# Performance work log

Measured on AMD Instinct MI355X. Metric: run time of the kernel, lower is better.

The kernel has to match this reference:

```python
import jax, jax.numpy as jnp
import numpy as np

B, N, D = 4, 4096, 256
DENSITY = 0.02


def setup_inputs() -> dict:
    key = jax.random.key(0)
    kx, ka1, ka2, kwt, kbt, kwh, kth = jax.random.split(key, 7)
    x = jax.random.normal(kx, (B, N, D), dtype=jnp.float32)
    # sparse weighted adjacency, materialized densely for the reference
    mask = jax.random.uniform(ka1, (B, N, N)) < DENSITY
    vals = jax.random.uniform(ka2, (B, N, N), dtype=jnp.float32)
    adj = jnp.where(mask, vals, 0.0).astype(jnp.float32)
    s = 0.02  # random_normal initializer stddev
    W_t = s * jax.random.normal(kwt, (D, D), dtype=jnp.float32)
    b_t = s * jax.random.normal(kbt, (D,), dtype=jnp.float32)
    W_h = s * jax.random.normal(kwh, (D, D), dtype=jnp.float32)
    theta = s * jax.random.normal(kth, (D, D), dtype=jnp.float32)
    return {"x": x, "adj": adj, "W_t": W_t, "b_t": b_t, "W_h": W_h, "theta": theta}


def reference(x, adj, W_t, b_t, W_h, theta):
    # degree normalization: norm = (deg + 1e-6)^{-1/2}
    in_degrees = jnp.sum(adj, axis=-1)                      # [B, N]
    norm = jnp.power(in_degrees + 1e-6, -0.5)[..., None]    # [B, N, 1]
    # homophilic path: D^{-1/2} A D^{-1/2} (x theta)
    f_hom = jnp.einsum('bnd,de->bne', x, theta) * norm      # [B, N, D]
    f_hom = jnp.einsum('bnm,bmd->bnd', adj, f_hom) * norm   # batched SpMM (dense ref)
    # heterophilic path
    f_het = jnp.einsum('bnd,de->bne', x, W_h)
    # gate and fuse
    gate = jax.nn.sigmoid(jnp.einsum('bnd,de->bne', x, W_t) + b_t)
    out = gate * f_hom + (1.0 - gate) * f_het
    return jax.nn.elu(out)
```

## Files before the change

kernel.cpp:

```cpp
#include <hip/hip_runtime.h>
#include <math.h>

constexpr int Nn = 4096;
constexpr int Dd = 256;
constexpr int Mrows = 16384;
constexpr int CAP = 192;
constexpr int GEMM_BLOCKS = 768;

typedef __attribute__((ext_vector_type(8))) short short8;
typedef __attribute__((ext_vector_type(4))) float f32x4;

__device__ __forceinline__ unsigned short f2bf(float f) {
    unsigned int u = __float_as_uint(f);
    u = (u + 0x7FFFu + ((u >> 16) & 1u)) >> 16;
    return (unsigned short)u;
}
__device__ __forceinline__ float bf2f(unsigned short u) {
    return __uint_as_float((unsigned int)u << 16);
}

__global__ __launch_bounds__(256) void prep_kernel(
    const float* __restrict__ x, const float* __restrict__ theta,
    const float* __restrict__ Wh, const float* __restrict__ Wt,
    unsigned short* __restrict__ xb, unsigned short* __restrict__ WT) {
    const int tid = threadIdx.x;
    if (blockIdx.x < 4096) {
        const size_t idx = (size_t)blockIdx.x * 1024 + tid * 4;
        float4 v = *(const float4*)(x + idx);
        ushort4 o;
        o.x = f2bf(v.x); o.y = f2bf(v.y); o.z = f2bf(v.z); o.w = f2bf(v.w);
        *(ushort4*)(xb + idx) = o;
    } else {
        const int b2 = blockIdx.x - 4096;
        const int m = b2 >> 8;
        const int c = b2 & 255;
        const float* src = (m == 0) ? theta : (m == 1 ? Wh : Wt);
        WT[(size_t)m * 65536 + (size_t)c * 256 + tid] = f2bf(src[(size_t)tid * 256 + c]);
    }
}

__global__ __launch_bounds__(256) void fused_kernel(
    const float* __restrict__ adj,
    const unsigned short* __restrict__ xb, const unsigned short* __restrict__ WT,
    const float* __restrict__ bt,
    float* __restrict__ norm, int* __restrict__ cntg, unsigned int* __restrict__ edges,
    unsigned short* __restrict__ T, float* __restrict__ H, float* __restrict__ G) {
    __shared__ __align__(16) char smraw[2 * 128 * 40 * 2];
    const int tid = threadIdx.x;

    if (blockIdx.x < GEMM_BLOCKS) {
        auto As = (unsigned short(*)[40])smraw;
        auto Bs = (unsigned short(*)[40])(smraw + 128 * 40 * 2);
        const int bid = blockIdx.x;
        const int rowbase = (bid & 127) * 128;
        const int y = bid >> 7;
        const int my = y >> 1;
        const int cb = (y & 1) * 128;
        const unsigned short* wm = WT + (size_t)my * 65536;

        const int l = tid & 63;
        const int w = tid >> 6;
        const int wr = w >> 1, wc = w & 1;
        const int l15 = l & 15, l4 = l >> 4;

        f32x4 acc[4][4];
#pragma unroll
        for (int m = 0; m < 4; ++m)
#pragma unroll
            for (int n = 0; n < 4; ++n) acc[m][n] = (f32x4)0.f;

        for (int k0 = 0; k0 < 256; k0 += 32) {
#pragma unroll
            for (int i = 0; i < 2; ++i) {
                const int c = tid + 256 * i;
                const int r = c >> 2, ko = (c & 3) * 8;
                *(int4*)&As[r][ko] = *(const int4*)(xb + (size_t)(rowbase + r) * 256 + k0 + ko);
                *(int4*)&Bs[r][ko] = *(const int4*)(wm + (size_t)(cb + r) * 256 + k0 + ko);
            }
            __syncthreads();
            short8 af[4], bf[4];
#pragma unroll
            for (int m = 0; m < 4; ++m) af[m] = *(short8*)&As[wr * 64 + m * 16 + l15][l4 * 8];
#pragma unroll
            for (int n = 0; n < 4; ++n) bf[n] = *(short8*)&Bs[wc * 64 + n * 16 + l15][l4 * 8];
#pragma unroll
            for (int m = 0; m < 4; ++m)
#pragma unroll
                for (int n = 0; n < 4; ++n)
                    acc[m][n] = __builtin_amdgcn_mfma_f32_16x16x32_bf16(af[m], bf[n], acc[m][n], 0, 0, 0);
            __syncthreads();
        }

#pragma unroll
        for (int m = 0; m < 4; ++m) {
#pragma unroll
            for (int n = 0; n < 4; ++n) {
                const int col = cb + wc * 64 + n * 16 + l15;
#pragma unroll
                for (int j = 0; j < 4; ++j) {
                    const int gr = rowbase + wr * 64 + m * 16 + l4 * 4 + j;
                    const size_t o = (size_t)gr * 256 + col;
                    const float v = acc[m][n][j];
                    if (my == 0) {
                        T[o] = f2bf(v);
                    } else if (my == 1) {
                        H[o] = v;
                    } else {
                        G[o] = 1.f / (1.f + expf(-(v + bt[col])));
                    }
                }
            }
        }
    } else {
        int* ml = (int*)smraw;
        float* vl = (float*)(smraw + CAP * 4);
        float* wsum = (float*)(smraw + CAP * 8);
        int* lcnt = (int*)(smraw + CAP * 8 + 16);
        const int row = blockIdx.x - GEMM_BLOCKS;
        if (tid == 0) *lcnt = 0;
        __syncthreads();

        const float* arow = adj + (size_t)row * Nn;
        float s = 0.f;
#pragma unroll
        for (int seg = 0; seg < 4; ++seg) {
            const int base = seg * 1024 + tid * 4;
            float4 v = *(const float4*)(arow + base);
            s += v.x + v.y + v.z + v.w;
            float vv[4] = {v.x, v.y, v.z, v.w};
#pragma unroll
            for (int j = 0; j < 4; ++j) {
                if (vv[j] != 0.f) {
                    int p = atomicAdd(lcnt, 1);
                    if (p < CAP) { ml[p] = base + j; vl[p] = vv[j]; }
                }
            }
        }
#pragma unroll
        for (int off = 32; off; off >>= 1) s += __shfl_down(s, off, 64);
        if ((tid & 63) == 0) wsum[tid >> 6] = s;
        __syncthreads();

        const int cc = min(*lcnt, CAP);
        if (tid == 0) {
            float d = wsum[0] + wsum[1] + wsum[2] + wsum[3];
            norm[row] = 1.0f / sqrtf(d + 1e-6f);
            cntg[row] = cc;
        }
        if (tid < cc) {
            edges[(size_t)row * CAP + tid] =
                ((unsigned int)ml[tid] << 16) | (unsigned int)f2bf(vl[tid]);
        }
    }
}

__global__ __launch_bounds__(256) void spmm_fuse_kernel(
    const int* __restrict__ cntg, const unsigned int* __restrict__ edges,
    const unsigned short* __restrict__ T, const float* __restrict__ H,
    const float* __restrict__ G, const float* __restrict__ norm,
    float* __restrict__ out) {
    const int bid = blockIdx.x;
    const int xcd = bid & 7;
    const int b = xcd >> 1;
    const int row = b * Nn + (xcd & 1) * 2048 + (bid >> 3);
    const int tid = threadIdx.x;

    __shared__ int sml[CAP];
    __shared__ float svl[CAP];

    const int c = cntg[row];
    if (tid < c) {
        const unsigned int pk = edges[(size_t)row * CAP + tid];
        const int m = (int)(pk >> 16);
        sml[tid] = m;
        svl[tid] = bf2f((unsigned short)(pk & 0xFFFFu)) * norm[b * Nn + m];
    }
    __syncthreads();

    const unsigned short* tb = T + (size_t)b * Nn * Dd;
    float a0 = 0.f, a1 = 0.f, a2 = 0.f, a3 = 0.f, a4 = 0.f, a5 = 0.f, a6 = 0.f, a7 = 0.f;
    int i = 0;
    for (; i + 8 <= c; i += 8) {
        a0 = fmaf(svl[i + 0], bf2f(tb[(size_t)sml[i + 0] * Dd + tid]), a0);
        a1 = fmaf(svl[i + 1], bf2f(tb[(size_t)sml[i + 1] * Dd + tid]), a1);
        a2 = fmaf(svl[i + 2], bf2f(tb[(size_t)sml[i + 2] * Dd + tid]), a2);
        a3 = fmaf(svl[i + 3], bf2f(tb[(size_t)sml[i + 3] * Dd + tid]), a3);
        a4 = fmaf(svl[i + 4], bf2f(tb[(size_t)sml[i + 4] * Dd + tid]), a4);
        a5 = fmaf(svl[i + 5], bf2f(tb[(size_t)sml[i + 5] * Dd + tid]), a5);
        a6 = fmaf(svl[i + 6], bf2f(tb[(size_t)sml[i + 6] * Dd + tid]), a6);
        a7 = fmaf(svl[i + 7], bf2f(tb[(size_t)sml[i + 7] * Dd + tid]), a7);
    }
    for (; i < c; ++i) a0 = fmaf(svl[i], bf2f(tb[(size_t)sml[i] * Dd + tid]), a0);
    const float acc = ((a0 + a1) + (a2 + a3)) + ((a4 + a5) + (a6 + a7));

    const float fh = acc * norm[row];
    const size_t o = (size_t)row * Dd + tid;
    const float g = G[o];
    const float h = H[o];
    const float val = g * fh + (1.f - g) * h;
    out[o] = val > 0.f ? val : expf(val) - 1.f;
}

extern "C" void kernel_launch(void* const* d_in, const int* in_sizes, int n_in,
                              void* d_out, int out_size, void* d_ws, size_t ws_size,
                              hipStream_t stream) {
    const float* x     = (const float*)d_in[0];
    const float* adj   = (const float*)d_in[1];
    const float* W_t   = (const float*)d_in[2];
    const float* b_t   = (const float*)d_in[3];
    const float* W_h   = (const float*)d_in[4];
    const float* theta = (const float*)d_in[5];
    float* out = (float*)d_out;

    char* p = (char*)d_ws;
    float* norm   = (float*)p;                 p += (size_t)Mrows * 4;
    int*   cntg   = (int*)p;                   p += (size_t)Mrows * 4;
    unsigned int* edges = (unsigned int*)p;    p += (size_t)Mrows * CAP * 4;
    unsigned short* xb = (unsigned short*)p;   p += (size_t)Mrows * Dd * 2;
    unsigned short* WT = (unsigned short*)p;   p += (size_t)3 * 256 * 256 * 2;
    unsigned short* T  = (unsigned short*)p;   p += (size_t)Mrows * Dd * 2;
    float* H = (float*)p;                      p += (size_t)Mrows * Dd * 4;
    float* G = (float*)p;

    prep_kernel<<<4096 + 768, 256, 0, stream>>>(x, theta, W_h, W_t, xb, WT);
    fused_kernel<<<GEMM_BLOCKS + Mrows, 256, 0, stream>>>(adj, xb, WT, b_t, norm, cntg,
                                                          edges, T, H, G);
    spmm_fuse_kernel<<<Mrows, 256, 0, stream>>>(cntg, edges, T, H, G, norm, out);
}
```

Baseline: 491.1 us.

## Process four rows per SpMM block with one wavefront per row and vector loads

The SpMM/fuse kernel now assigns four output rows to each block, one 64-lane wavefront per row, and each lane handles four feature columns. Gathers change from 2-byte to 8-byte loads, and the epilogue uses float4 loads and stores. Edge weights are pre-scaled by the neighbor norm and repacked as bf16 in shared memory, which drops the separate index and value arrays. The aim is fewer blocks, wider memory transactions and less per-row overhead. The cost is extra rounding of the scaled weight to bf16 and possible load imbalance when the four rows have different degrees.

```diff
diff --git a/kernel.cpp b/kernel.cpp
--- a/kernel.cpp
+++ b/kernel.cpp
@@ -162,43 +162,84 @@
     const int bid = blockIdx.x;
     const int xcd = bid & 7;
     const int b = xcd >> 1;
-    const int row = b * Nn + (xcd & 1) * 2048 + (bid >> 3);
+    const int rowbase = b * Nn + (xcd & 1) * 2048 + (bid >> 3) * 4;
     const int tid = threadIdx.x;
-
-    __shared__ int sml[CAP];
-    __shared__ float svl[CAP];
-
-    const int c = cntg[row];
-    if (tid < c) {
-        const unsigned int pk = edges[(size_t)row * CAP + tid];
-        const int m = (int)(pk >> 16);
-        sml[tid] = m;
-        svl[tid] = bf2f((unsigned short)(pk & 0xFFFFu)) * norm[b * Nn + m];
-    }
+    const int w = tid >> 6;
+    const int l = tid & 63;
+
+    __shared__ unsigned int sedge[4][CAP];
+    __shared__ int scnt[4];
+
+    if (tid < 4) scnt[tid] = cntg[rowbase + tid];
     __syncthreads();
-
-    const unsigned short* tb = T + (size_t)b * Nn * Dd;
-    float a0 = 0.f, a1 = 0.f, a2 = 0.f, a3 = 0.f, a4 = 0.f, a5 = 0.f, a6 = 0.f, a7 = 0.f;
+    {
+        const int r = tid >> 6, e0 = tid & 63;
+        const int c = scnt[r];
+        const float* nb = norm + b * Nn;
+        const unsigned int* erow = edges + (size_t)(rowbase + r) * CAP;
+#pragma unroll
+        for (int it = 0; it < 3; ++it) {
+            const int e = e0 + it * 64;
+            if (e < c) {
+                const unsigned int pk = erow[e];
+                const int m = (int)(pk >> 16);
+                const float v = __uint_as_float(pk << 16) * nb[m];
+                sedge[r][e] = ((unsigned int)m << 16) | (unsigned int)f2bf(v);
+            }
+        }
+    }
+    __syncthreads();
+
+    const int c = scnt[w];
+    const unsigned int* el = sedge[w];
+    const unsigned short* tl = T + (size_t)b * Nn * Dd + l * 4;
+
+    float4 a0 = {0.f, 0.f, 0.f, 0.f}, a1 = a0, a2 = a0, a3 = a0;
     int i = 0;
     for (; i + 8 <= c; i += 8) {
-        a0 = fmaf(svl[i + 0], bf2f(tb[(size_t)sml[i + 0] * Dd + tid]), a0);
-        a1 = fmaf(svl[i + 1], bf2f(tb[(size_t)sml[i + 1] * Dd + tid]), a1);
-        a2 = fmaf(svl[i + 2], bf2f(tb[(size_t)sml[i + 2] * Dd + tid]), a2);
-        a3 = fmaf(svl[i + 3], bf2f(tb[(size_t)sml[i + 3] * Dd + tid]), a3);
-        a4 = fmaf(svl[i + 4], bf2f(tb[(size_t)sml[i + 4] * Dd + tid]), a4);
-        a5 = fmaf(svl[i + 5], bf2f(tb[(size_t)sml[i + 5] * Dd + tid]), a5);
-        a6 = fmaf(svl[i + 6], bf2f(tb[(size_t)sml[i + 6] * Dd + tid]), a6);
-        a7 = fmaf(svl[i + 7], bf2f(tb[(size_t)sml[i + 7] * Dd + tid]), a7);
-    }
-    for (; i < c; ++i) a0 = fmaf(svl[i], bf2f(tb[(size_t)sml[i] * Dd + tid]), a0);
-    const float acc = ((a0 + a1) + (a2 + a3)) + ((a4 + a5) + (a6 + a7));
-
-    const float fh = acc * norm[row];
-    const size_t o = (size_t)row * Dd + tid;
-    const float g = G[o];
-    const float h = H[o];
-    const float val = g * fh + (1.f - g) * h;
-    out[o] = val > 0.f ? val : expf(val) - 1.f;
+        const unsigned int p0 = el[i + 0], p1 = el[i + 1], p2 = el[i + 2], p3 = el[i + 3];
+        const unsigned int p4 = el[i + 4], p5 = el[i + 5], p6 = el[i + 6], p7 = el[i + 7];
+        const uint2 d0 = *(const uint2*)(tl + (p0 >> 16) * 256);
+        const uint2 d1 = *(const uint2*)(tl + (p1 >> 16) * 256);
+        const uint2 d2 = *(const uint2*)(tl + (p2 >> 16) * 256);
+        const uint2 d3 = *(const uint2*)(tl + (p3 >> 16) * 256);
+        const uint2 d4 = *(const uint2*)(tl + (p4 >> 16) * 256);
+        const uint2 d5 = *(const uint2*)(tl + (p5 >> 16) * 256);
+        const uint2 d6 = *(const uint2*)(tl + (p6 >> 16) * 256);
+        const uint2 d7 = *(const uint2*)(tl + (p7 >> 16) * 256);
+#define ACC(A, P, DW)                                                        \
+        {                                                                    \
+            const float vf = __uint_as_float((P) << 16);                     \
+            A.x = fmaf(vf, __uint_as_float((DW).x << 16), A.x);              \
+            A.y = fmaf(vf, __uint_as_float((DW).x & 0xFFFF0000u), A.y);      \
+            A.z = fmaf(vf, __uint_as_float((DW).y << 16), A.z);              \
+            A.w = fmaf(vf, __uint_as_float((DW).y & 0xFFFF0000u), A.w);      \
+        }
+        ACC(a0, p0, d0) ACC(a1, p1, d1) ACC(a2, p2, d2) ACC(a3, p3, d3)
+        ACC(a0, p4, d4) ACC(a1, p5, d5) ACC(a2, p6, d6) ACC(a3, p7, d7)
+    }
+    for (; i < c; ++i) {
+        const unsigned int p0 = el[i];
+        const uint2 d0 = *(const uint2*)(tl + (p0 >> 16) * 256);
+        ACC(a0, p0, d0)
+    }
+#undef ACC
+
+    const int row = rowbase + w;
+    const float nr = norm[row];
+    const size_t o = (size_t)row * 256 + l * 4;
+    const float4 g = *(const float4*)(G + o);
+    const float4 h = *(const float4*)(H + o);
+    float4 r;
+    r.x = g.x * ((a0.x + a1.x + a2.x + a3.x) * nr) + (1.f - g.x) * h.x;
+    r.y = g.y * ((a0.y + a1.y + a2.y + a3.y) * nr) + (1.f - g.y) * h.y;
+    r.z = g.z * ((a0.z + a1.z + a2.z + a3.z) * nr) + (1.f - g.z) * h.z;
+    r.w = g.w * ((a0.w + a1.w + a2.w + a3.w) * nr) + (1.f - g.w) * h.w;
+    r.x = r.x > 0.f ? r.x : expf(r.x) - 1.f;
+    r.y = r.y > 0.f ? r.y : expf(r.y) - 1.f;
+    r.z = r.z > 0.f ? r.z : expf(r.z) - 1.f;
+    r.w = r.w > 0.f ? r.w : expf(r.w) - 1.f;
+    *(float4*)(out + o) = r;
 }
 
 extern "C" void kernel_launch(void* const* d_in, const int* in_sizes, int n_in,
@@ -225,5 +266,5 @@
     prep_kernel<<<4096 + 768, 256, 0, stream>>>(x, theta, W_h, W_t, xb, WT);
     fused_kernel<<<GEMM_BLOCKS + Mrows, 256, 0, stream>>>(adj, xb, WT, b_t, norm, cntg,
                                                           edges, T, H, G);
-    spmm_fuse_kernel<<<Mrows, 256, 0, stream>>>(cntg, edges, T, H, G, norm, out);
-}
+    spmm_fuse_kernel<<<Mrows / 4, 256, 0, stream>>>(cntg, edges, T, H, G, norm, out);
+}
```

Measured after the change: 479.5 us. 1.02x faster.
